# Kernel tuning notes

Hardware: AMD Instinct MI355X
Metric: run time of the kernel (lower is better)

## Reference

```python
import jax, jax.numpy as jnp
import numpy as np
from jax import lax

DN = ('NDHWC', 'DHWIO', 'NDHWC')
SHAPE = (33, 33, 33)
B = 2
N = 40000
C = 64


def setup_inputs() -> dict:
    key = jax.random.key(0)
    ks = jax.random.split(key, 24)
    D, H, W = SHAPE
    # unique active voxel coords (batch, z, y, x)
    rng = np.random.default_rng(0)
    idx = rng.choice(B * D * H * W, size=N, replace=False)
    b = idx // (D * H * W)
    r = idx % (D * H * W)
    coors = np.stack([b, r // (H * W), (r // W) % H, r % W], axis=1).astype(np.int32)

    def w(k, shape, scale=0.1):
        return jax.random.normal(k, shape, jnp.float32) * scale

    inp = {
        'features': jax.random.normal(ks[0], (N, 3), jnp.float32),
        'coors': jnp.asarray(coors),
        'batch_size': B,
        'w1': w(ks[1], (3, 3, 3, 3, C), 0.2), 'b1': w(ks[2], (C,), 0.05),
        'w2': w(ks[3], (3, 3, 3, C, C), 0.05), 'b2': w(ks[4], (C,), 0.05),
        'w3': w(ks[5], (3, 3, 3, C, C), 0.05), 'b3': w(ks[6], (C,), 0.05),
        'wt': w(ks[7], (3, 3, 3, C, C), 0.05), 'bt': w(ks[8], (C,), 0.05),
        'w5': w(ks[9], (3, 3, 3, C, C), 0.05), 'b5': w(ks[10], (C,), 0.05),
    }
    # folded eval-mode BatchNorm: y = x*s + h  (s = gamma/sqrt(var+eps), h = beta - mean*s)
    for i, (sk, hk) in enumerate(zip(ks[11:16], ks[16:21]), start=1):
        inp[f's{i}'] = 1.0 + 0.1 * jax.random.normal(sk, (C,), jnp.float32)
        inp[f'h{i}'] = 0.05 * jax.random.normal(hk, (C,), jnp.float32)
    return inp


def _forward(features, coors, batch_size,
             w1, b1, w2, b2, w3, b3, wt, bt, w5, b5,
             s1, h1, s2, h2, s3, h3, s4, h4, s5, h5):
    D, H, W = SHAPE
    bi, zi, yi, xi = coors[:, 0], coors[:, 1], coors[:, 2], coors[:, 3]
    # densify SparseConvTensor (zeros at inactive sites) + active mask
    x = jnp.zeros((batch_size, D, H, W, features.shape[-1]), features.dtype)
    x = x.at[bi, zi, yi, xi].set(features)
    m = jnp.zeros((batch_size, D, H, W, 1), jnp.float32).at[bi, zi, yi, xi].set(1.0)
    ones3 = jnp.ones((3, 3, 3, 1, 1), jnp.float32)

    conv = lambda a, k, pad: lax.conv_general_dilated(a, k, (1, 1, 1), pad, dimension_numbers=DN)
    # masked BN(eval) + ReLU: applied only on active sites, background stays exactly 0
    act = lambda y, mm, s, h: jnp.where(mm, jax.nn.relu(y * s + h), 0.0)

    # SparseConv3d(3,64,3): valid conv; output actives = 1-dilation of input actives
    x = conv(x, w1, 'VALID')
    m1 = conv(m, ones3, 'VALID') > 0  # [B,31,31,31,1]
    x = act(x + b1, m1, s1, h1)

    # two SubMConv3d(64,64,3) sharing indice_key: same active set, SAME padding
    x = act(conv(x, w2, 'SAME') + b2, m1, s2, h2)
    x = act(conv(x, w3, 'SAME') + b3, m1, s3, h3)

    # SparseConvTranspose3d(64,64,3,2): out = (D-1)*2+3; actives = transposed dilation
    x = lax.conv_transpose(x, wt, (2, 2, 2), 'VALID', dimension_numbers=DN)
    mT = lax.conv_transpose(m1.astype(jnp.float32), ones3, (2, 2, 2), 'VALID', dimension_numbers=DN) > 0
    x = act(x + bt, mT, s4, h4)

    # ToDense -> dense Conv3d(64,64,3) -> BN -> ReLU (dense: applied everywhere)
    x = conv(x, w5, 'VALID') + b5
    x = jax.nn.relu(x * s5 + h5)
    return jnp.transpose(x, (0, 4, 1, 2, 3))  # NCDHW like spconv ToDense output


def reference(features, coors, batch_size,
              w1, b1, w2, b2, w3, b3, wt, bt, w5, b5,
              s1, h1, s2, h2, s3, h3, s4, h4, s5, h5):
    return _forward(features, coors, batch_size,
                    w1, b1, w2, b2, w3, b3, wt, bt, w5, b5,
                    s1, h1, s2, h2, s3, h3, s4, h4, s5, h5)
```

## Files before the change

kernel.cpp:

```cpp
#include <hip/hip_runtime.h>
#include <cstdint>

constexpr int BB = 2, C = 64;
constexpr int D1 = 31;
constexpr int DP = 33;
constexpr int D4 = 63;
constexpr int D5 = 61;
constexpr int D5CUBE = D5*D5*D5;

constexpr int NV1 = BB*D1*D1*D1;
constexpr int NVP = BB*DP*DP*DP;
constexpr int NV4 = BB*D4*D4*D4;
constexpr int NV5 = BB*D5*D5*D5;

constexpr size_t alup(size_t x) { return (x + 255) & ~(size_t)255; }
constexpr size_t OB_X0  = 0;
constexpr size_t OB_M0  = alup(OB_X0  + (size_t)NVP*3*4);
constexpr size_t OB_M1P = alup(OB_M0  + (size_t)NVP*4);
constexpr size_t OB_X1  = alup(OB_M1P + (size_t)NVP*4);
constexpr size_t OB_X2  = alup(OB_X1  + (size_t)NVP*64*2);
constexpr size_t OB_X3  = alup(OB_X2  + (size_t)NVP*64*2);
constexpr size_t OB_X4  = alup(OB_X3  + (size_t)NVP*64*2);
constexpr size_t OB_WB2 = alup(OB_X4  + (size_t)NV4*64*2);
constexpr size_t OB_WB3 = alup(OB_WB2 + (size_t)27*64*64*2);
constexpr size_t OB_WBT = alup(OB_WB3 + (size_t)27*64*64*2);
constexpr size_t OB_WB5 = alup(OB_WBT + (size_t)27*64*64*2);

typedef __attribute__((ext_vector_type(8))) short short8;
typedef __attribute__((ext_vector_type(4))) float f32x4;

__device__ inline unsigned short f2bf(float f) {
  unsigned int u = __float_as_uint(f);
  u = (u + 0x7FFFu + ((u >> 16) & 1u)) >> 16;
  return (unsigned short)u;
}

template<int DD>
__device__ inline void decodev(int vox, int& b, int& z, int& y, int& x) {
  x = vox % DD; int r = vox / DD;
  y = r % DD;   r /= DD;
  z = r % DD;   b = r / DD;
}

__device__ inline int xcd_swz(int bid, int nb) {
  int q = nb >> 3, r = nb & 7;
  int xcd = bid & 7, idx = bid >> 3;
  return (xcd < r ? xcd*(q+1) : r*(q+1) + (xcd - r)*q) + idx;
}

constexpr int SETUP_ZBLK = (NVP + 255) / 256;

__global__ void __launch_bounds__(256)
k_setup(float* __restrict__ x0, float* __restrict__ m0, float* __restrict__ m1p,
        unsigned short* __restrict__ x1, unsigned short* __restrict__ x2,
        unsigned short* __restrict__ x3,
        const float* __restrict__ wa, const float* __restrict__ wb,
        const float* __restrict__ wc, const float* __restrict__ wd,
        unsigned short* __restrict__ da, unsigned short* __restrict__ db,
        unsigned short* __restrict__ dc, unsigned short* __restrict__ dd) {
  if (blockIdx.x < SETUP_ZBLK) {
    int v = blockIdx.x*256 + threadIdx.x;
    if (v >= NVP) return;
    m0[v] = 0.f; m1p[v] = 0.f;
    x0[3*v+0] = 0.f; x0[3*v+1] = 0.f; x0[3*v+2] = 0.f;
    int x = v % DP, r = v / DP;
    int y = r % DP; r /= DP;
    int z = r % DP;
    if (x==0 || x==DP-1 || y==0 || y==DP-1 || z==0 || z==DP-1) {
      ulonglong2 zz = {0ull, 0ull};
      ulonglong2* p1 = (ulonglong2*)(x1 + (size_t)v*64);
      ulonglong2* p2 = (ulonglong2*)(x2 + (size_t)v*64);
      ulonglong2* p3 = (ulonglong2*)(x3 + (size_t)v*64);
      #pragma unroll
      for (int i = 0; i < 8; i++) { p1[i] = zz; p2[i] = zz; p3[i] = zz; }
    }
  } else {
    int rblk = blockIdx.x - SETUP_ZBLK;
    int which = rblk / 432;
    int i = (rblk - which*432)*256 + threadIdx.x;
    const float* w = which == 0 ? wa : which == 1 ? wb : which == 2 ? wc : wd;
    unsigned short* dst = which == 0 ? da : which == 1 ? db : which == 2 ? dc : dd;
    int co = i & 63, k = (i >> 6) & 63, t = i >> 12;
    int kk = k >> 5, q = (k >> 3) & 3, j = k & 7, cb = co >> 4, l = q*16 + (co & 15);
    dst[(size_t)((t*2+kk)*4+cb)*512 + l*8 + j] = f2bf(w[i]);
  }
}

__global__ void k_scatter(const float* __restrict__ feat, const int* __restrict__ coors,
                          int n, float* __restrict__ x0, float* __restrict__ m0) {
  int i = blockIdx.x*blockDim.x + threadIdx.x;
  if (i >= n) return;
  int b = coors[4*i+0], z = coors[4*i+1], y = coors[4*i+2], x = coors[4*i+3];
  int v = ((b*DP + z)*DP + y)*DP + x;
  x0[v*3+0] = feat[3*i+0];
  x0[v*3+1] = feat[3*i+1];
  x0[v*3+2] = feat[3*i+2];
  m0[v] = 1.0f;
}

__global__ void __launch_bounds__(256)
k_conv1(const float* __restrict__ x0, const float* __restrict__ m0,
        unsigned short* __restrict__ x1, float* __restrict__ m1p,
        const float* __restrict__ w1, const float* __restrict__ b1,
        const float* __restrict__ s1, const float* __restrict__ h1) {
  long long t = (long long)blockIdx.x*blockDim.x + threadIdx.x;
  if (t >= (long long)NV1*C) return;
  int co  = (int)(t & 63);
  int vox = (int)(t >> 6);
  int b, z, y, x; decodev<D1>(vox, b, z, y, x);
  float sum = 0.f, mm = 0.f;
  #pragma unroll
  for (int kz=0; kz<3; kz++)
  #pragma unroll
  for (int ky=0; ky<3; ky++)
  #pragma unroll
  for (int kx=0; kx<3; kx++) {
    int iv = ((b*DP + z+kz)*DP + y+ky)*DP + (x+kx);
    mm += m0[iv];
    const float* px = x0 + iv*3;
    const float* pw = w1 + ((kz*3+ky)*3+kx)*3*64 + co;
    sum += px[0]*pw[0] + px[1]*pw[64] + px[2]*pw[128];
  }
  bool m = mm > 0.f;
  float o = m ? fmaxf((sum + b1[co])*s1[co] + h1[co], 0.f) : 0.f;
  size_t pOff = (size_t)(((b*DP + z+1)*DP + y+1)*DP + (x+1));
  x1[pOff*C + co] = f2bf(o);
  if (co == 0) m1p[pOff] = m ? 1.f : 0.f;
}

__device__ __forceinline__ void c_step2(const short8 (&A)[2], const short8 (&W)[4],
                                        f32x4 (&acc)[2][4]) {
  #pragma unroll
  for (int a = 0; a < 2; a++)
    #pragma unroll
    for (int cb = 0; cb < 4; cb++)
      acc[a][cb] = __builtin_amdgcn_mfma_f32_16x16x32_bf16(W[cb], A[a], acc[a][cb], 0, 0, 0);
}

__device__ __forceinline__ void c5_step(const short8 (&A)[4], const short8 (&W)[4],
                                        f32x4 (&acc)[4][4]) {
  #pragma unroll
  for (int a = 0; a < 4; a++)
    #pragma unroll
    for (int cb = 0; cb < 4; cb++)
      acc[a][cb] = __builtin_amdgcn_mfma_f32_16x16x32_bf16(W[cb], A[a], acc[a][cb], 0, 0, 0);
}

constexpr int C23_HALF = 1280;

__global__ void __launch_bounds__(256)
k_conv23_mfma(const unsigned short* __restrict__ xin, const unsigned short* __restrict__ wB,
              unsigned short* __restrict__ xout, const float* __restrict__ m1p,
              const float* __restrict__ bias, const float* __restrict__ s,
              const float* __restrict__ h) {
  __shared__ short8 sA[2*C23_HALF];
  const int tid  = threadIdx.x;
  const int lane = tid & 63;
  const int wid  = tid >> 6;
  const int ll   = lane & 15;
  const int l16  = lane >> 4;

  const int blk = xcd_swz(blockIdx.x, gridDim.x);
  const int yt  = blk & 7;
  const int rzb = blk >> 3;
  const int z   = rzb % D1;
  const int b   = rzb / D1;
  const int y0  = yt * 4;

  int st_r[5], st_base[5];
  #pragma unroll
  for (int it = 0; it < 5; ++it) {
    int g = it*256 + tid; g = g > 1055 ? 1055 : g;
    int r = g / 264, rem = g - r*264;
    int v = rem >> 3, c16p = rem & 7;
    int c16l = c16p ^ (v & 7);
    st_r[it] = r;
    st_base[it] = (v << 7) + (c16l << 4);
  }

  const char* xinb = (const char*)xin;

  f32x4 acc[2][4];
  #pragma unroll
  for (int a = 0; a < 2; a++)
    #pragma unroll
    for (int cb = 0; cb < 4; cb++)
      acc[a][cb] = f32x4{0.f, 0.f, 0.f, 0.f};

  auto STAGE = [&](int kzn, int kyn, int hn) {
    size_t pb = (size_t)((b*DP + z + kzn)*DP) * (DP*128);
    char* dst = (char*)&sA[0] + hn*(C23_HALF*16);
    #pragma unroll
    for (int it = 0; it < 5; ++it) {
      int yin = y0 + st_r[it] + kyn; yin = yin > 32 ? 32 : yin;
      __builtin_amdgcn_global_load_lds(
        (const __attribute__((address_space(1))) void*)(xinb + pb + (size_t)yin*(DP*128) + st_base[it]),
        (__attribute__((address_space(3))) void*)(dst + it*4096 + wid*1024),
        16, 0, 0);
    }
  };
  auto LDA = [&](int hh, int kx, int kk, short8 (&A)[2]) {
    #pragma unroll
    for (int a = 0; a < 2; a++) {
      int xv = a*16 + ll; xv = xv > 30 ? 30 : xv;
      int v  = xv + kx;
      int ch = hh*C23_HALF + wid*264 + v*8 + ((kk*4 + l16) ^ (v & 7));
      A[a] = sA[ch];
    }
  };

  short8 A0[2], A1[2];

  STAGE(0, 0, 0);
  __syncthreads();

  int kzn = 0, kyn = 1;
  #pragma unroll 1
  for (int p = 0; p < 9; ++p) {
    const int hh = p & 1;

    short8 W[6][4];
    {
      const unsigned short* wp = wB + (size_t)p*12288 + lane*8;
      #pragma unroll
      for (int st = 0; st < 6; ++st)
        #pragma unroll
        for (int cb = 0; cb < 4; cb++)
          W[st][cb] = *reinterpret_cast<const short8*>(wp + st*2048 + cb*512);
    }
    __builtin_amdgcn_sched_barrier(0);

    if (p < 8) {
      STAGE(kzn, kyn, hh ^ 1);
      kyn++; if (kyn == 3) { kyn = 0; kzn++; }
    }
    __builtin_amdgcn_sched_barrier(0);

    LDA(hh, 0, 0, A0);
    #pragma unroll
    for (int st = 0; st < 6; ++st) {
      const int kxn = (st+1) >> 1, kkn = (st+1) & 1;
      if (st < 5) {
        if (st & 1) LDA(hh, kxn, kkn, A0); else LDA(hh, kxn, kkn, A1);
      }
      if (st & 1) c_step2(A1, W[st], acc); else c_step2(A0, W[st], acc);
    }
    __syncthreads();
  }

  const int y = y0 + wid;
  if (y < D1) {
    #pragma unroll
    for (int a = 0; a < 2; a++) {
      int x = a*16 + ll;
      if (x >= D1) continue;
      size_t pOff = (size_t)(((b*DP + z+1)*DP + y+1)*DP + (x+1));
      bool m = m1p[pOff] > 0.f;
      #pragma unroll
      for (int cb = 0; cb < 4; cb++) {
        unsigned long long pack = 0;
        #pragma unroll
        for (int r = 0; r < 4; r++) {
          int co = cb*16 + l16*4 + r;
          float o = m ? fmaxf((acc[a][cb][r] + bias[co])*s[co] + h[co], 0.f) : 0.f;
          pack |= (unsigned long long)f2bf(o) << (16*r);
        }
        *reinterpret_cast<unsigned long long*>(xout + pOff*64 + cb*16 + l16*4) = pack;
      }
    }
  }
}

constexpr int CT_CHUNKS = 1792;

__global__ void __launch_bounds__(256)
k_convT_mfma(const unsigned short* __restrict__ x3, const unsigned short* __restrict__ wB,
             unsigned short* __restrict__ x4, const float* __restrict__ m1p,
             const float* __restrict__ bias, const float* __restrict__ s,
             const float* __restrict__ h) {
  __shared__ short8 sb[CT_CHUNKS];
  __shared__ float sMask[4*64];
  const int tid  = threadIdx.x;
  const int lane = tid & 63;
  const int wid  = tid >> 6;
  const int ii   = lane & 15;
  const int l16  = lane >> 4;

  const int blk   = xcd_swz(blockIdx.x, gridDim.x);
  const int ytile = blk & 15;
  const int rzb   = blk >> 4;
  const int zo    = rzb % D4;
  const int b     = rzb / D4;
  const int y0    = ytile * 4;

  const int izp0 = (zo + (zo & 1)) >> 1;
  const int izp1 = (zo & 1) ? izp0 : izp0 + 1;

  #pragma unroll
  for (int it = 0; it < 7; ++it) {
    int g = it*256 + tid; g = g > 1583 ? 1583 : g;
    int r6 = g / 264, rem = g - r6*264;
    int v = rem >> 3, c16p = rem & 7;
    int c16l = c16p ^ (v & 7);
    int pz  = r6 >= 3 ? 1 : 0;
    int ry  = r6 - pz*3;
    int izp = pz ? izp1 : izp0;
    int iyp = ytile*2 + ry;
    size_t srcB = ((size_t)((b*DP + izp)*DP + iyp)*DP)*128 + (size_t)(v << 7) + (c16l << 4);
    __builtin_amdgcn_global_load_lds(
      (const __attribute__((address_space(1))) void*)((const char*)x3 + srcB),
      (__attribute__((address_space(3))) void*)((char*)&sb[0] + it*4096 + wid*1024),
      16, 0, 0);
  }

  {
    const int yo_m = y0 + wid;
    const int xo_m = lane > 62 ? 62 : lane;
    float mm = 0.f;
    #pragma unroll
    for (int kz = 0; kz < 3; kz++) {
      if ((zo + kz) & 1) continue;
      int izp = ((zo + kz - 2) >> 1) + 1;
      #pragma unroll
      for (int ky = 0; ky < 3; ky++) {
        if ((yo_m + ky) & 1) continue;
        int iyp = ((yo_m + ky - 2) >> 1) + 1;
        #pragma unroll
        for (int kx = 0; kx < 3; kx++) {
          if ((xo_m + kx) & 1) continue;
          int ixp = ((xo_m + kx - 2) >> 1) + 1;
          mm += m1p[((b*DP + izp)*DP + iyp)*DP + ixp];
        }
      }
    }
    sMask[wid*64 + lane] = mm;
  }
  __syncthreads();

  f32x4 acc[4][4];
  #pragma unroll
  for (int a = 0; a < 4; a++)
    #pragma unroll
    for (int cb = 0; cb < 4; cb++)
      acc[a][cb] = f32x4{0.f, 0.f, 0.f, 0.f};

  const int yo = y0 + wid;
  if (yo < D4) {
    const int nPz = (zo & 1) ? 1 : 2;
    #pragma unroll 1
    for (int pz = 0; pz < 2; ++pz) {
      if (pz >= nPz) break;
      const int kz = (zo & 1) ? 1 : pz*2;
      #pragma unroll 1
      for (int kyi = 0; kyi < 2; ++kyi) {
        int ky, ry;
        if (wid & 1) { if (kyi == 1) break; ky = 1; ry = (wid + 1) >> 1; }
        else         { ky = kyi*2;          ry = (wid >> 1) + kyi; }
        const int rbase = (pz*3 + ry)*264;
        #pragma unroll
        for (int kx = 0; kx < 3; ++kx) {
          const int apar  = kx & 1;
          const int xoffE = ((kx + apar - 2) >> 1) + 1;
          const int t = (kz*3 + ky)*3 + kx;
          #pragma unroll
          for (int kk = 0; kk < 2; ++kk) {
            short8 Bv[4];
            const unsigned short* wpk = wB + (size_t)(t*2+kk)*2048 + lane*8;
            #pragma unroll
            for (int cb = 0; cb < 4; cb++)
              Bv[cb] = *reinterpret_cast<const short8*>(wpk + cb*512);
            #pragma unroll
            for (int ablk = 0; ablk < 2; ablk++) {
              const int ixp = ablk*16 + ii + xoffE;
              short8 A = sb[rbase + ixp*8 + ((kk*4 + l16) ^ (ixp & 7))];
              const int afr = apar*2 + ablk;
              #pragma unroll
              for (int cb = 0; cb < 4; cb++)
                acc[afr][cb] = __builtin_amdgcn_mfma_f32_16x16x32_bf16(A, Bv[cb], acc[afr][cb], 0, 0, 0);
            }
          }
        }
      }
    }

    float bv[4], sv[4], hv[4];
    #pragma unroll
    for (int cb = 0; cb < 4; cb++) {
      int c = cb*16 + (lane & 15);
      bv[cb] = bias[c]; sv[cb] = s[c]; hv[cb] = h[c];
    }
    const int rowBase = ((b*D4 + zo)*D4 + yo)*D4;
    #pragma unroll
    for (int a = 0; a < 4; a++) {
      const int ablk = a & 1, apar = a >> 1;
      #pragma unroll
      for (int r = 0; r < 4; r++) {
        const int row = (lane >> 4)*4 + r;
        const int xo  = 2*(ablk*16 + row) + apar;
        if (xo >= D4) continue;
        const int vox = rowBase + xo;
        const bool m = sMask[wid*64 + xo] > 0.f;
        #pragma unroll
        for (int cb = 0; cb < 4; cb++) {
          float o = m ? fmaxf((acc[a][cb][r] + bv[cb])*sv[cb] + hv[cb], 0.f) : 0.f;
          x4[(size_t)vox*64 + cb*16 + (lane & 15)] = f2bf(o);
        }
      }
    }
  }
}

constexpr int C5_WSLOT = 544;

__global__ void __launch_bounds__(256, 2)
k_conv5_mfma(const unsigned short* __restrict__ x4, const unsigned short* __restrict__ wB,
             float* __restrict__ out, const float* __restrict__ bias,
             const float* __restrict__ s, const float* __restrict__ h) {
  __shared__ short8 sA[2*4*C5_WSLOT];
  const int tid  = threadIdx.x;
  const int lane = tid & 63;
  const int wid  = tid >> 6;
  const int ll   = lane & 15;
  const int l16  = lane >> 4;

  const int blk   = xcd_swz(blockIdx.x, gridDim.x);
  const int ytile = blk & 15;
  const int rzb   = blk >> 4;
  const int z     = rzb % D5;
  const int b     = rzb / D5;
  const int y0    = ytile * 4;

  int st_off[8];
  #pragma unroll
  for (int it = 0; it < 8; ++it) {
    int g = it*64 + lane; g = g > 503 ? 503 : g;
    int v = g >> 3, c16p = g & 7;
    int c16l = c16p ^ (v & 7);
    st_off[it] = (v << 7) + (c16l << 4);
  }

  const char* x4b = (const char*)x4;

  f32x4 acc[4][4];
  #pragma unroll
  for (int a = 0; a < 4; a++)
    #pragma unroll
    for (int cb = 0; cb < 4; cb++)
      acc[a][cb] = f32x4{0.f, 0.f, 0.f, 0.f};

  auto STAGE = [&](int kzn, int kyn, int hn) {
    int yin = y0 + wid + kyn; yin = yin > 62 ? 62 : yin;
    size_t rb = ((size_t)((b*D4 + z + kzn)*D4 + yin)) * 8064;
    char* dst = (char*)&sA[0] + (size_t)(hn*4 + wid)*(C5_WSLOT*16);
    #pragma unroll
    for (int it = 0; it < 8; ++it) {
      __builtin_amdgcn_global_load_lds(
        (const __attribute__((address_space(1))) void*)(x4b + rb + st_off[it]),
        (__attribute__((address_space(3))) void*)(dst + it*1024),
        16, 0, 0);
    }
  };
  auto LDA = [&](int hh, int kx, int kk, short8 (&A)[4]) {
    #pragma unroll
    for (int a = 0; a < 4; a++) {
      int v  = a*16 + ll + kx;
      int ch = (hh*4 + wid)*C5_WSLOT + v*8 + ((kk*4 + l16) ^ (v & 7));
      A[a] = sA[ch];
    }
  };

  short8 A0[4], A1[4], A2[4];

  STAGE(0, 0, 0);

#define C5_BODY(p0,p1,p2,p3,p4,p5)                                    \
  do {                                                                 \
    LDA(hh, (p0)>>1, (p0)&1, A0);                                      \
    LDA(hh, (p1)>>1, (p1)&1, A1);                                      \
    LDA(hh, (p2)>>1, (p2)&1, A2);  c5_step(A0, W[p0], acc);            \
    LDA(hh, (p3)>>1, (p3)&1, A0);  c5_step(A1, W[p1], acc);            \
    LDA(hh, (p4)>>1, (p4)&1, A1);  c5_step(A2, W[p2], acc);            \
    LDA(hh, (p5)>>1, (p5)&1, A2);  c5_step(A0, W[p3], acc);            \
    c5_step(A1, W[p4], acc);                                           \
    c5_step(A2, W[p5], acc);                                           \
  } while (0)

  int kzn = 0, kyn = 1;
  #pragma unroll 1
  for (int p = 0; p < 9; ++p) {
    const int hh = p & 1;

    short8 W[6][4];
    {
      const unsigned short* wp = wB + (size_t)p*12288 + lane*8;
      #pragma unroll
      for (int st = 0; st < 6; ++st)
        #pragma unroll
        for (int cb = 0; cb < 4; cb++)
          W[st][cb] = *reinterpret_cast<const short8*>(wp + st*2048 + cb*512);
    }
    __builtin_amdgcn_sched_barrier(0);

    if (p < 8) {
      STAGE(kzn, kyn, hh ^ 1);
      kyn++; if (kyn == 3) { kyn = 0; kzn++; }
    } else {
      STAGE(2, 2, hh ^ 1);
    }
    __builtin_amdgcn_sched_barrier(0);

    asm volatile("s_waitcnt vmcnt(32)" ::: "memory");
    __builtin_amdgcn_sched_barrier(0);

    C5_BODY(0,1,2,3,4,5);
  }
#undef C5_BODY

  const int yout = y0 + wid;
  if (yout < D5) {
    #pragma unroll
    for (int a = 0; a < 4; a++) {
      int x = a*16 + ll;
      if (x >= D5) continue;
      size_t sp = (size_t)(z*D5 + yout)*D5 + x;
      #pragma unroll
      for (int cb = 0; cb < 4; cb++)
        #pragma unroll
        for (int r = 0; r < 4; r++) {
          int co = cb*16 + l16*4 + r;
          float o = fmaxf((acc[a][cb][r] + bias[co])*s[co] + h[co], 0.f);
          out[(size_t)(b*64 + co)*D5CUBE + sp] = o;
        }
    }
  }
}

extern "C" void kernel_launch(void* const* d_in, const int* in_sizes, int n_in,
                              void* d_out, int out_size, void* d_ws, size_t ws_size,
                              hipStream_t stream) {
  const float* feat  = (const float*)d_in[0];
  const int*   coors = (const int*)d_in[1];
  const float* w1 = (const float*)d_in[3];
  const float* b1 = (const float*)d_in[4];
  const float* w2 = (const float*)d_in[5];
  const float* b2 = (const float*)d_in[6];
  const float* w3 = (const float*)d_in[7];
  const float* b3 = (const float*)d_in[8];
  const float* wt = (const float*)d_in[9];
  const float* bt = (const float*)d_in[10];
  const float* w5 = (const float*)d_in[11];
  const float* b5 = (const float*)d_in[12];
  const float* s1 = (const float*)d_in[13];
  const float* h1 = (const float*)d_in[14];
  const float* s2 = (const float*)d_in[15];
  const float* h2 = (const float*)d_in[16];
  const float* s3 = (const float*)d_in[17];
  const float* h3 = (const float*)d_in[18];
  const float* s4 = (const float*)d_in[19];
  const float* h4 = (const float*)d_in[20];
  const float* s5 = (const float*)d_in[21];
  const float* h5 = (const float*)d_in[22];
  int n = in_sizes[0] / 3;

  char* wsb = (char*)d_ws;
  float*          X0  = (float*)(wsb + OB_X0);
  float*          M0  = (float*)(wsb + OB_M0);
  float*          M1P = (float*)(wsb + OB_M1P);
  unsigned short* X1  = (unsigned short*)(wsb + OB_X1);
  unsigned short* X2  = (unsigned short*)(wsb + OB_X2);
  unsigned short* X3  = (unsigned short*)(wsb + OB_X3);
  unsigned short* X4  = (unsigned short*)(wsb + OB_X4);
  unsigned short* WB2 = (unsigned short*)(wsb + OB_WB2);
  unsigned short* WB3 = (unsigned short*)(wsb + OB_WB3);
  unsigned short* WBT = (unsigned short*)(wsb + OB_WBT);
  unsigned short* WB5 = (unsigned short*)(wsb + OB_WB5);

  k_setup<<<SETUP_ZBLK + 1728, 256, 0, stream>>>(X0, M0, M1P, X1, X2, X3,
                                                 w2, w3, wt, w5, WB2, WB3, WBT, WB5);

  k_scatter<<<(n+255)/256, 256, 0, stream>>>(feat, coors, n, X0, M0);

  {
    long long threads = (long long)NV1*C;
    k_conv1<<<(int)((threads+255)/256), 256, 0, stream>>>(X0, M0, X1, M1P, w1, b1, s1, h1);
  }

  constexpr int BLK23 = BB * D1 * 8;
  k_conv23_mfma<<<BLK23, 256, 0, stream>>>(X1, WB2, X2, M1P, b2, s2, h2);
  k_conv23_mfma<<<BLK23, 256, 0, stream>>>(X2, WB3, X3, M1P, b3, s3, h3);

  constexpr int BLK_T = BB * D4 * 16;
  k_convT_mfma<<<BLK_T, 256, 0, stream>>>(X3, WBT, X4, M1P, bt, s4, h4);

  constexpr int BLK5 = BB * D5 * 16;
  k_conv5_mfma<<<BLK5, 256, 0, stream>>>(X4, WB5, (float*)d_out, b5, s5, h5);
}
```

Baseline: 311.2 us.

## Stage full 3x6-row input halo into LDS once, drop double-buffered pipeline in conv23

The conv2/conv3 MFMA kernel now loads the whole halo it needs (3 z-planes by 6 y-rows by 33 x by 64 channels) into LDS in one pass, then runs all 27 taps with a single barrier. This replaces the 9-step double-buffered staging loop and its per-step barriers. LDS use grows from about 40KB to about 76KB per block, which can cut occupancy. Weights are now loaded per tap right before use instead of prefetched six steps at a time, and all global-memory latency is exposed up front with nothing overlapping it.

```diff
diff --git a/kernel.cpp b/kernel.cpp
--- a/kernel.cpp
+++ b/kernel.cpp
@@ -146,14 +146,14 @@
       acc[a][cb] = __builtin_amdgcn_mfma_f32_16x16x32_bf16(W[cb], A[a], acc[a][cb], 0, 0, 0);
 }
 
-constexpr int C23_HALF = 1280;
+constexpr int C23_CHUNKS = 4864;
 
 __global__ void __launch_bounds__(256)
 k_conv23_mfma(const unsigned short* __restrict__ xin, const unsigned short* __restrict__ wB,
               unsigned short* __restrict__ xout, const float* __restrict__ m1p,
               const float* __restrict__ bias, const float* __restrict__ s,
               const float* __restrict__ h) {
-  __shared__ short8 sA[2*C23_HALF];
+  __shared__ short8 sA[C23_CHUNKS];
   const int tid  = threadIdx.x;
   const int lane = tid & 63;
   const int wid  = tid >> 6;
@@ -167,18 +167,21 @@
   const int b   = rzb / D1;
   const int y0  = yt * 4;
 
-  int st_r[5], st_base[5];
-  #pragma unroll
-  for (int it = 0; it < 5; ++it) {
-    int g = it*256 + tid; g = g > 1055 ? 1055 : g;
-    int r = g / 264, rem = g - r*264;
+  #pragma unroll
+  for (int it = 0; it < 19; ++it) {
+    int g = it*256 + tid; g = g > 4751 ? 4751 : g;
+    int r18 = g / 264, rem = g - r18*264;
     int v = rem >> 3, c16p = rem & 7;
     int c16l = c16p ^ (v & 7);
-    st_r[it] = r;
-    st_base[it] = (v << 7) + (c16l << 4);
-  }
-
-  const char* xinb = (const char*)xin;
+    int pz = r18 / 6, r = r18 - pz*6;
+    int iyp = y0 + r; iyp = iyp > 32 ? 32 : iyp;
+    size_t srcB = ((size_t)((b*DP + z + pz)*DP + iyp)*DP)*128 + (size_t)(v << 7) + (c16l << 4);
+    __builtin_amdgcn_global_load_lds(
+      (const __attribute__((address_space(1))) void*)((const char*)xin + srcB),
+      (__attribute__((address_space(3))) void*)((char*)&sA[0] + it*4096 + wid*1024),
+      16, 0, 0);
+  }
+  __syncthreads();
 
   f32x4 acc[2][4];
   #pragma unroll
@@ -187,65 +190,27 @@
     for (int cb = 0; cb < 4; cb++)
       acc[a][cb] = f32x4{0.f, 0.f, 0.f, 0.f};
 
-  auto STAGE = [&](int kzn, int kyn, int hn) {
-    size_t pb = (size_t)((b*DP + z + kzn)*DP) * (DP*128);
-    char* dst = (char*)&sA[0] + hn*(C23_HALF*16);
-    #pragma unroll
-    for (int it = 0; it < 5; ++it) {
-      int yin = y0 + st_r[it] + kyn; yin = yin > 32 ? 32 : yin;
-      __builtin_amdgcn_global_load_lds(
-        (const __attribute__((address_space(1))) void*)(xinb + pb + (size_t)yin*(DP*128) + st_base[it]),
-        (__attribute__((address_space(3))) void*)(dst + it*4096 + wid*1024),
-        16, 0, 0);
-    }
-  };
-  auto LDA = [&](int hh, int kx, int kk, short8 (&A)[2]) {
-    #pragma unroll
-    for (int a = 0; a < 2; a++) {
-      int xv = a*16 + ll; xv = xv > 30 ? 30 : xv;
-      int v  = xv + kx;
-      int ch = hh*C23_HALF + wid*264 + v*8 + ((kk*4 + l16) ^ (v & 7));
-      A[a] = sA[ch];
-    }
-  };
-
-  short8 A0[2], A1[2];
-
-  STAGE(0, 0, 0);
-  __syncthreads();
-
-  int kzn = 0, kyn = 1;
   #pragma unroll 1
-  for (int p = 0; p < 9; ++p) {
-    const int hh = p & 1;
-
-    short8 W[6][4];
-    {
-      const unsigned short* wp = wB + (size_t)p*12288 + lane*8;
-      #pragma unroll
-      for (int st = 0; st < 6; ++st)
-        #pragma unroll
-        for (int cb = 0; cb < 4; cb++)
-          W[st][cb] = *reinterpret_cast<const short8*>(wp + st*2048 + cb*512);
-    }
-    __builtin_amdgcn_sched_barrier(0);
-
-    if (p < 8) {
-      STAGE(kzn, kyn, hh ^ 1);
-      kyn++; if (kyn == 3) { kyn = 0; kzn++; }
-    }
-    __builtin_amdgcn_sched_barrier(0);
-
-    LDA(hh, 0, 0, A0);
-    #pragma unroll
-    for (int st = 0; st < 6; ++st) {
-      const int kxn = (st+1) >> 1, kkn = (st+1) & 1;
-      if (st < 5) {
-        if (st & 1) LDA(hh, kxn, kkn, A0); else LDA(hh, kxn, kkn, A1);
+  for (int t = 0; t < 27; ++t) {
+    const int kz = t / 9, rr = t - kz*9;
+    const int ky = rr / 3, kx = rr - ky*3;
+    const int rbase = (kz*6 + wid + ky)*264;
+    #pragma unroll
+    for (int kk = 0; kk < 2; ++kk) {
+      short8 Bv[4];
+      const unsigned short* wp = wB + (size_t)(t*2+kk)*2048 + lane*8;
+      #pragma unroll
+      for (int cb = 0; cb < 4; cb++)
+        Bv[cb] = *reinterpret_cast<const short8*>(wp + cb*512);
+      short8 A[2];
+      #pragma unroll
+      for (int a = 0; a < 2; a++) {
+        int xv = a*16 + ll; xv = xv > 30 ? 30 : xv;
+        int v  = xv + kx;
+        A[a] = sA[rbase + v*8 + ((kk*4 + l16) ^ (v & 7))];
       }
-      if (st & 1) c_step2(A1, W[st], acc); else c_step2(A0, W[st], acc);
-    }
-    __syncthreads();
+      c_step2(A, Bv, acc);
+    }
   }
 
   const int y = y0 + wid;
```

After: 312.1 us. Within noise of the previous version (+0.3%).
